# Performance work log

Hardware: AMD Instinct MI355X
Metric: run time of the kernel (lower is better)

Reference implementation:

```python
import jax, jax.numpy as jnp
import numpy as np

EPS = 1e-5

def setup_inputs() -> dict:
    key = jax.random.key(0)
    ks = jax.random.split(key, 7)
    C = 512
    x = jax.random.normal(ks[0], (16, C, 32, 32), dtype=jnp.float32)
    gn_w = jax.random.normal(ks[1], (C,), dtype=jnp.float32) * 0.02 + 1.0
    gn_b = jax.random.normal(ks[2], (C,), dtype=jnp.float32) * 0.02
    qkv_w = jax.random.normal(ks[3], (3 * C, C), dtype=jnp.float32) * (1.0 / np.sqrt(C))
    qkv_b = jax.random.normal(ks[4], (3 * C,), dtype=jnp.float32) * 0.02
    proj_w = jax.random.normal(ks[5], (C, C), dtype=jnp.float32) * (1.0 / np.sqrt(C))
    proj_b = jax.random.normal(ks[6], (C,), dtype=jnp.float32) * 0.02
    return {"x": x, "gn_w": gn_w, "gn_b": gn_b, "qkv_w": qkv_w,
            "qkv_b": qkv_b, "proj_w": proj_w, "proj_b": proj_b}

def reference(x, gn_w, gn_b, qkv_w, qkv_b, proj_w, proj_b):
    B, C, H, W = x.shape
    S = H * W
    # GroupNorm with 1 group: normalize over (C,H,W) per sample
    mean = jnp.mean(x, axis=(1, 2, 3), keepdims=True)
    var = jnp.var(x, axis=(1, 2, 3), keepdims=True)
    h = (x - mean) * jax.lax.rsqrt(var + EPS)
    h = h * gn_w[None, :, None, None] + gn_b[None, :, None, None]
    # 1x1 conv qkv: [B,C,H,W] -> [B,3C,H,W], flatten spatial -> [B,S,3C]
    hf = h.reshape(B, C, S)  # b c s
    qkv = jnp.einsum('bcs,oc->bso', hf, qkv_w) + qkv_b  # [B,S,3C]
    q, k, v = jnp.split(qkv, 3, axis=-1)  # each [B,S,C]
    scale = C ** (-0.5)
    attn = jax.nn.softmax(jnp.einsum('bqc,bkc->bqk', q, k) * scale, axis=-1)
    out = jnp.einsum('bqk,bkc->bqc', attn, v)  # [B,S,C]
    out = jnp.einsum('bsc,oc->bso', out, proj_w) + proj_b
    out = out.transpose(0, 2, 1).reshape(B, C, H, W)
    return x + out
```

## Files before the change

kernel.cpp:

```cpp
#include <hip/hip_runtime.h>
#include <stdint.h>

#define B_  16
#define C_  512
#define S_  1024
#define NSAMP (C_*S_)

typedef __bf16 bf16x8 __attribute__((ext_vector_type(8)));
typedef float  f32x4  __attribute__((ext_vector_type(4)));

__device__ __forceinline__ float bf2f(uint16_t u){ return __uint_as_float(((uint32_t)u)<<16); }
__device__ __forceinline__ uint16_t f2bf(float f){
  uint32_t u = __float_as_uint(f);
  uint32_t r = u + 0x7fffu + ((u>>16)&1u);
  return (uint16_t)(r>>16);
}
__device__ __forceinline__ float wsum(float v){
  #pragma unroll
  for(int o=32;o;o>>=1) v += __shfl_xor(v,o,64);
  return v;
}
__device__ __forceinline__ void gload16(const void* g, void* l){
  __builtin_amdgcn_global_load_lds(
      (__attribute__((address_space(1))) void*)g,
      (__attribute__((address_space(3))) void*)l, 16, 0, 0);
}

__global__ __launch_bounds__(1024) void detect_k(const uint16_t* __restrict__ x,
                                                 int* __restrict__ flag){
  __shared__ int sh[16];
  const uint4* xv = (const uint4*)x;
  int cnt = 0;
  #pragma unroll
  for(int k=0;k<8;k++){
    uint4 v = xv[threadIdx.x + k*1024];
    uint32_t ww[4] = {v.x, v.y, v.z, v.w};
    #pragma unroll
    for(int q=0;q<4;q++){
      cnt += (((ww[q] & 0xffffu) >> 7) & 0xffu) >= 132 ? 1 : 0;
      cnt += (((ww[q] >> 16)     >> 7) & 0xffu) >= 132 ? 1 : 0;
    }
  }
  #pragma unroll
  for(int o=32;o;o>>=1) cnt += __shfl_xor(cnt,o,64);
  const int lane = threadIdx.x & 63, w = threadIdx.x >> 6;
  if (lane==0) sh[w] = cnt;
  __syncthreads();
  if (threadIdx.x==0){
    int tot = 0;
    #pragma unroll
    for(int i=0;i<16;i++) tot += sh[i];
    *flag = (tot > 4096) ? 1 : 0;
  }
}

__device__ __forceinline__ void convseg(const void* src, uint16_t* dst, int n, int f, int t){
  const int idx = t*8;
  if (idx >= n) return;
  if (f){
    const float* s = (const float*)src;
    float4 v0 = *(const float4*)(s + idx);
    float4 v1 = *(const float4*)(s + idx + 4);
    ushort4 a, b;
    a.x=f2bf(v0.x); a.y=f2bf(v0.y); a.z=f2bf(v0.z); a.w=f2bf(v0.w);
    b.x=f2bf(v1.x); b.y=f2bf(v1.y); b.z=f2bf(v1.z); b.w=f2bf(v1.w);
    *(ushort4*)(dst + idx)     = a;
    *(ushort4*)(dst + idx + 4) = b;
  } else {
    *(uint4*)(dst + idx) = *(const uint4*)((const uint16_t*)src + idx);
  }
}
__global__ __launch_bounds__(256) void prep_k(
    const void* __restrict__ srcx, uint16_t* __restrict__ xb, float2* __restrict__ part,
    const void* qkvw, const void* projw, const void* gnw, const void* gnb,
    const void* qkvb, const void* projb,
    uint16_t* qkvwb, uint16_t* projwb, uint16_t* gnwb, uint16_t* gnbb,
    uint16_t* qkvbb, uint16_t* projbb, const int* __restrict__ flag){
  const int f = *flag;
  const int t = threadIdx.x;
  if (blockIdx.x >= 1024){
    const int bid = blockIdx.x - 1024;
    if (bid < 384){
      const size_t off = (size_t)bid*2048;
      convseg((const char*)qkvw + off*(f?4:2), qkvwb + off, 2048, f, t);
    } else if (bid < 512){
      const size_t off = (size_t)(bid-384)*2048;
      convseg((const char*)projw + off*(f?4:2), projwb + off, 2048, f, t);
    } else {
      convseg(gnw,   gnwb,   512,  f, t);
      convseg(gnb,   gnbb,   512,  f, t);
      convseg(qkvb,  qkvbb,  1536, f, t);
      convseg(projb, projbb, 512,  f, t);
    }
    return;
  }
  const size_t base = (size_t)blockIdx.x * 8192;
  float s = 0.f, s2 = 0.f;
  if (f){
    const float4* sp = (const float4*)((const float*)srcx + base);
    ushort4* dp = (ushort4*)(xb + base);
    #pragma unroll
    for(int i=0;i<8;i++){
      float4 v = sp[i*256 + t];
      s  += v.x + v.y + v.z + v.w;
      s2 += v.x*v.x + v.y*v.y + v.z*v.z + v.w*v.w;
      ushort4 o; o.x=f2bf(v.x); o.y=f2bf(v.y); o.z=f2bf(v.z); o.w=f2bf(v.w);
      dp[i*256 + t] = o;
    }
  } else {
    const uint4* sp = (const uint4*)((const uint16_t*)srcx + base);
    uint4* dp = (uint4*)(xb + base);
    #pragma unroll
    for(int i=0;i<4;i++){
      uint4 p = sp[i*256 + t];
      dp[i*256 + t] = p;
      uint32_t uu[4] = {p.x,p.y,p.z,p.w};
      #pragma unroll
      for(int q=0;q<4;q++){
        float f0 = __uint_as_float(uu[q]<<16);
        float f1 = __uint_as_float(uu[q] & 0xffff0000u);
        s += f0 + f1; s2 += f0*f0 + f1*f1;
      }
    }
  }
  s = wsum(s); s2 = wsum(s2);
  __shared__ float rs[4], rq[4];
  const int lane = t & 63, w = t >> 6;
  if (lane==0){ rs[w]=s; rq[w]=s2; }
  __syncthreads();
  if (t==0)
    part[blockIdx.x] = make_float2(rs[0]+rs[1]+rs[2]+rs[3], rq[0]+rq[1]+rq[2]+rq[3]);
}

__global__ __launch_bounds__(256) void gn_apply_t(const uint16_t* __restrict__ x,
    const uint16_t* __restrict__ gw, const uint16_t* __restrict__ gb,
    const float2* __restrict__ part, uint16_t* __restrict__ hT){
  __shared__ float tile[64*129];
  const int b = blockIdx.z, c0 = blockIdx.y<<6, s0 = blockIdx.x<<7;
  const int t = threadIdx.x;
  float2 p = part[b*64 + (t & 63)];
  float s = wsum(p.x), s2 = wsum(p.y);
  const float ninv = 1.f/(float)NSAMP;
  const float mn = s*ninv;
  const float rstd = rsqrtf(s2*ninv - mn*mn + 1e-5f);
  #pragma unroll
  for(int k=0;k<4;k++){
    const int ci = t + k*256;
    const int cl = ci>>4, sc = ci&15;
    uint4 v = *(const uint4*)&x[((size_t)b*C_ + c0+cl)*S_ + s0 + sc*8];
    const uint16_t* e = (const uint16_t*)&v;
    float* dst = &tile[cl*129 + sc*8];
    #pragma unroll
    for(int q=0;q<8;q++) dst[q] = bf2f(e[q]);
  }
  __syncthreads();
  const int cc = t & 7;
  const int sb0 = t >> 3;
  uint4 wv4 = *(const uint4*)&gw[c0 + cc*8];
  uint4 bv4 = *(const uint4*)&gb[c0 + cc*8];
  const uint16_t* we = (const uint16_t*)&wv4;
  const uint16_t* be = (const uint16_t*)&bv4;
  float aq[8], cq[8];
  #pragma unroll
  for(int q=0;q<8;q++){ aq[q] = bf2f(we[q])*rstd; cq[q] = bf2f(be[q]) - mn*aq[q]; }
  #pragma unroll
  for(int k=0;k<4;k++){
    const int sl = sb0 + k*32;
    uint16_t ov[8];
    #pragma unroll
    for(int q=0;q<8;q++){
      float xv = tile[(cc*8+q)*129 + sl];
      ov[q] = f2bf(xv*aq[q] + cq[q]);
    }
    uint4 o;
    o.x = (uint32_t)ov[0] | ((uint32_t)ov[1]<<16);
    o.y = (uint32_t)ov[2] | ((uint32_t)ov[3]<<16);
    o.z = (uint32_t)ov[4] | ((uint32_t)ov[5]<<16);
    o.w = (uint32_t)ov[6] | ((uint32_t)ov[7]<<16);
    *(uint4*)&hT[((size_t)b*S_ + s0+sl)*C_ + c0 + cc*8] = o;
  }
}

__global__ __launch_bounds__(256)
void qkv_k(const uint16_t* __restrict__ hT, const uint16_t* __restrict__ qkvw,
           const uint16_t* __restrict__ qkvb, uint16_t* __restrict__ qk,
           uint16_t* __restrict__ Vt)
{
  __shared__ uint16_t smem[16384];
  uint16_t* As = smem;
  uint16_t* Bs = smem + 8192;
  const int tid = threadIdx.x;
  const int lane = tid & 63, w = tid >> 6;
  const int quad = lane >> 4, lm = lane & 15;
  const int wm = (w & 1) << 6, wn = (w >> 1) << 6;

  const bool vpath = blockIdx.x >= 1024;
  const int id = vpath ? (blockIdx.x - 1024) : blockIdx.x;
  const int r8 = id & 7, k8 = id >> 3;
  int m0, n0, bz;
  const uint16_t *Abase, *Bbase;
  if (!vpath){
    const int g = r8*16 + (k8 & 15);
    m0 = g << 7; n0 = (k8 >> 4) << 7; bz = 0;
    Abase = hT + (size_t)m0*512;
    Bbase = qkvw + (size_t)n0*512;
  } else {
    const int g = r8*16 + (k8 & 15);
    m0 = (k8 >> 4) << 7; n0 = (g & 7) << 7; bz = g >> 3;
    Abase = qkvw + (size_t)(1024 + m0)*512;
    Bbase = hT + (size_t)bz*S_*C_ + (size_t)n0*512;
  }

  f32x4 acc[4][4];
  #pragma unroll
  for(int i=0;i<4;i++)
    #pragma unroll
    for(int j=0;j<4;j++) acc[i][j] = (f32x4){0.f,0.f,0.f,0.f};

  const int srow = tid >> 3;
  const int sx   = (tid & 7) ^ (srow & 7);
  const uint16_t* ga = Abase + (size_t)srow*512 + sx*8;
  const uint16_t* gb = Bbase + (size_t)srow*512 + sx*8;
  uint16_t* sa = &As[tid*8];
  uint16_t* sb = &Bs[tid*8];

  for(int k0=0;k0<512;k0+=64){
    #pragma unroll
    for(int i=0;i<4;i++){
      gload16(ga + (size_t)(i*32)*512 + k0, sa + i*2048);
      gload16(gb + (size_t)(i*32)*512 + k0, sb + i*2048);
    }
    __syncthreads();
    #pragma unroll
    for(int kk=0;kk<64;kk+=32){
      bf16x8 av[4], bv[4];
      #pragma unroll
      for(int i=0;i<4;i++){
        const int row = wm + i*16 + lm;
        av[i] = *(const bf16x8*)&As[row*64 + ((((kk>>3)+quad) ^ (row&7))<<3)];
      }
      #pragma unroll
      for(int j=0;j<4;j++){
        const int row = wn + j*16 + lm;
        bv[j] = *(const bf16x8*)&Bs[row*64 + ((((kk>>3)+quad) ^ (row&7))<<3)];
      }
      #pragma unroll
      for(int i=0;i<4;i++)
        #pragma unroll
        for(int j=0;j<4;j++)
          acc[i][j] = __builtin_amdgcn_mfma_f32_16x16x32_bf16(av[i], bv[j], acc[i][j], 0,0,0);
    }
    __syncthreads();
  }

  uint16_t* Cs = smem;
  if (!vpath){
    #pragma unroll
    for(int j=0;j<4;j++){
      const int col_l = wn + j*16 + lm;
      const float bvv = bf2f(qkvb[n0 + col_l]);
      #pragma unroll
      for(int i=0;i<4;i++){
        const int rl0 = wm + i*16 + (quad<<2);
        #pragma unroll
        for(int r=0;r<4;r++)
          Cs[(rl0+r)*128 + col_l] = f2bf(acc[i][j][r] + bvv);
      }
    }
  } else {
    #pragma unroll
    for(int i=0;i<4;i++){
      const int rl0 = wm + i*16 + (quad<<2);
      #pragma unroll
      for(int r=0;r<4;r++){
        const float bvv = bf2f(qkvb[1024 + m0 + rl0 + r]);
        #pragma unroll
        for(int j=0;j<4;j++)
          Cs[(rl0+r)*128 + wn + j*16 + lm] = f2bf(acc[i][j][r] + bvv);
      }
    }
  }
  __syncthreads();
  uint16_t* base = vpath ? (Vt + (size_t)bz*C_*S_) : qk;
  #pragma unroll
  for(int k=0;k<8;k++){
    const int ci = tid + k*256;
    const int rl = ci>>4, ccc = ci&15;
    *(uint4*)&base[(size_t)(m0+rl)*1024 + n0 + ccc*8] = *(const uint4*)&Cs[rl*128 + ccc*8];
  }
}

template<bool HASBIAS, bool BIASROW, bool OUTDYN, bool HASRES, int SWZMODE, bool EXP, bool SUMNORM>
__global__ __launch_bounds__(256)
void gemm_bt(const uint16_t* __restrict__ A, const uint16_t* __restrict__ Bt,
             void* __restrict__ Cp, const uint16_t* __restrict__ bias,
             const uint16_t* __restrict__ xres, const int* __restrict__ flag,
             int lda, int ldb, int ldc, int K,
             long long sA, long long sB, long long sC)
{
  __shared__ uint16_t smem[16384];
  uint16_t* As = smem;
  uint16_t* Bs = smem + 8192;
  const int lin = (blockIdx.z * gridDim.y + blockIdx.y) * gridDim.x + blockIdx.x;
  const int r8 = lin & 7, kk8 = lin >> 3;
  int bx, by, bz;
  if (SWZMODE == 0){
    const int G = (gridDim.y * gridDim.z) >> 3;
    const int g = r8 * G + (kk8 % G);
    bx = kk8 / G; by = g % gridDim.y; bz = g / gridDim.y;
  } else {
    const int G = (gridDim.x * gridDim.z) >> 3;
    const int g = r8 * G + (kk8 % G);
    by = kk8 / G; bx = g % gridDim.x; bz = g / gridDim.x;
  }

  const int tid = threadIdx.x;
  const int lane = tid & 63, w = tid >> 6;
  const int quad = lane >> 4, lm = lane & 15;
  const int m0 = by << 7, n0 = bx << 7;
  A  += (size_t)bz * sA;
  Bt += (size_t)bz * sB;

  f32x4 acc[4][4];
  #pragma unroll
  for(int i=0;i<4;i++)
    #pragma unroll
    for(int j=0;j<4;j++) acc[i][j] = (f32x4){0.f,0.f,0.f,0.f};
  f32x4 rsum[4];
  bf16x8 onesv;
  if (SUMNORM){
    #pragma unroll
    for(int i=0;i<4;i++) rsum[i] = (f32x4){0.f,0.f,0.f,0.f};
    #pragma unroll
    for(int z=0;z<8;z++) onesv[z] = (__bf16)1.0f;
  }

  const int wm = (w & 1) << 6, wn = (w >> 1) << 6;
  const int srow = tid >> 3;
  const int sx   = (tid & 7) ^ (srow & 7);
  const uint16_t* ga = A  + (size_t)(m0 + srow)*lda + sx*8;
  const uint16_t* gb = Bt + (size_t)(n0 + srow)*ldb + sx*8;
  uint16_t* sa = &As[tid*8];
  uint16_t* sb = &Bs[tid*8];

  for(int k0=0;k0<K;k0+=64){
    #pragma unroll
    for(int i=0;i<4;i++){
      gload16(ga + (size_t)(i*32)*lda + k0, sa + i*2048);
      gload16(gb + (size_t)(i*32)*ldb + k0, sb + i*2048);
    }
    __syncthreads();
    #pragma unroll
    for(int kk=0;kk<64;kk+=32){
      bf16x8 av[4], bv[4];
      #pragma unroll
      for(int i=0;i<4;i++){
        const int row = wm + i*16 + lm;
        av[i] = *(const bf16x8*)&As[row*64 + ((((kk>>3)+quad) ^ (row&7))<<3)];
      }
      #pragma unroll
      for(int j=0;j<4;j++){
        const int row = wn + j*16 + lm;
        bv[j] = *(const bf16x8*)&Bs[row*64 + ((((kk>>3)+quad) ^ (row&7))<<3)];
      }
      #pragma unroll
      for(int i=0;i<4;i++){
        if (SUMNORM) rsum[i] = __builtin_amdgcn_mfma_f32_16x16x32_bf16(av[i], onesv, rsum[i], 0,0,0);
        #pragma unroll
        for(int j=0;j<4;j++)
          acc[i][j] = __builtin_amdgcn_mfma_f32_16x16x32_bf16(av[i], bv[j], acc[i][j], 0,0,0);
      }
    }
    __syncthreads();
  }

  const size_t cb = (size_t)bz * (size_t)sC;
  if (!OUTDYN && !HASRES){
    uint16_t* Cs = smem;
    #pragma unroll
    for(int j=0;j<4;j++){
      const int col_l = wn + j*16 + lm;
      const float cbias = (HASBIAS && !BIASROW) ? bf2f(bias[n0 + col_l]) : 0.f;
      #pragma unroll
      for(int i=0;i<4;i++){
        const int rl0 = wm + i*16 + (quad<<2);
        #pragma unroll
        for(int r=0;r<4;r++){
          float v = acc[i][j][r] + cbias;
          if (HASBIAS && BIASROW) v += bf2f(bias[m0 + rl0 + r]);
          if (EXP)     v = __expf(v * 0.044194173824159216f);
          if (SUMNORM) v = v / rsum[i][r];
          Cs[(rl0+r)*128 + col_l] = f2bf(v);
        }
      }
    }
    __syncthreads();
    uint16_t* base = (uint16_t*)Cp + cb;
    #pragma unroll
    for(int k=0;k<8;k++){
      const int ci = tid + k*256;
      const int rl = ci>>4, cc = ci&15;
      *(uint4*)&base[(size_t)(m0+rl)*ldc + n0 + cc*8] = *(const uint4*)&Cs[rl*128 + cc*8];
    }
  } else {
    float* Cs32 = (float*)smem;
    const int f = OUTDYN ? *flag : 0;
    const int wnh = wn >> 1;
    #pragma unroll
    for(int half=0; half<2; ++half){
      #pragma unroll
      for(int j2=0;j2<2;j2++){
        const int j = half*2 + j2;
        const int col_l = wn + j*16 + lm;
        const int hcol = wnh + j2*16 + lm;
        const float cbias = (HASBIAS && !BIASROW) ? bf2f(bias[n0 + col_l]) : 0.f;
        #pragma unroll
        for(int i=0;i<4;i++){
          const int rl0 = wm + i*16 + (quad<<2);
          #pragma unroll
          for(int r=0;r<4;r++){
            float v = acc[i][j][r] + cbias;
            if (HASBIAS && BIASROW) v += bf2f(bias[m0 + rl0 + r]);
            if (EXP)     v = __expf(v * 0.044194173824159216f);
            if (SUMNORM) v = v / rsum[i][r];
            Cs32[(rl0+r)*64 + hcol] = v;
          }
        }
      }
      __syncthreads();
      #pragma unroll
      for(int k=0;k<8;k++){
        const int ci = tid + k*256;
        const int rl = ci>>4, c4 = ci&15;
        float4 vv = *(const float4*)&Cs32[rl*64 + c4*4];
        const int gcol = n0 + c4*4 + ((c4>=8)?32:0) + half*32;
        const size_t idx = cb + (size_t)(m0+rl)*ldc + gcol;
        float o0=vv.x, o1=vv.y, o2=vv.z, o3=vv.w;
        if (HASRES){
          uint2 rr = *(const uint2*)&xres[idx];
          o0 += bf2f((uint16_t)(rr.x & 0xffffu));
          o1 += bf2f((uint16_t)(rr.x >> 16));
          o2 += bf2f((uint16_t)(rr.y & 0xffffu));
          o3 += bf2f((uint16_t)(rr.y >> 16));
        }
        if (OUTDYN && f){
          float4 o = make_float4(o0,o1,o2,o3);
          *(float4*)&((float*)Cp)[idx] = o;
        } else {
          uint2 o;
          o.x = (uint32_t)f2bf(o0) | ((uint32_t)f2bf(o1)<<16);
          o.y = (uint32_t)f2bf(o2) | ((uint32_t)f2bf(o3)<<16);
          *(uint2*)&((uint16_t*)Cp)[idx] = o;
        }
      }
      __syncthreads();
    }
  }
}

extern "C" void kernel_launch(void* const* d_in, const int* in_sizes, int n_in,
                              void* d_out, int out_size, void* d_ws, size_t ws_size,
                              hipStream_t stream){
  char* ws = (char*)d_ws;
  int*      flag  = (int*)ws;
  float2*   part  = (float2*)(ws + 4096);
  uint16_t* gnwb  = (uint16_t*)(ws + 16384);
  uint16_t* gnbb  = (uint16_t*)(ws + 17408);
  uint16_t* qkvbb = (uint16_t*)(ws + 18432);
  uint16_t* projbb= (uint16_t*)(ws + 21504);
  uint16_t* qkvwb = (uint16_t*)(ws + 32768);
  uint16_t* projwb= (uint16_t*)(ws + 1605632);
  uint16_t* xb    = (uint16_t*)(ws + 4194304);
  uint16_t* hT    = (uint16_t*)(ws + 20971520);
  uint16_t* qk    = (uint16_t*)(ws + 37748736);
  uint16_t* sc    = (uint16_t*)(ws + 71303168);
  uint16_t* Vt    = (uint16_t*)(ws + 104857600);

  hipLaunchKernelGGL(detect_k, dim3(1), dim3(1024), 0, stream,
                     (const uint16_t*)d_in[0], flag);
  hipLaunchKernelGGL(prep_k, dim3(1537), dim3(256), 0, stream,
                     d_in[0], xb, part,
                     d_in[3], d_in[5], d_in[1], d_in[2], d_in[4], d_in[6],
                     qkvwb, projwb, gnwb, gnbb, qkvbb, projbb, flag);
  hipLaunchKernelGGL(gn_apply_t, dim3(8,8,16), dim3(256), 0, stream, xb, gnwb, gnbb, part, hT);

  hipLaunchKernelGGL(qkv_k, dim3(1536), dim3(256), 0, stream, hT, qkvwb, qkvbb, qk, Vt);

  hipLaunchKernelGGL((gemm_bt<false,false,false,false,0,true,false>), dim3(8,8,16), dim3(256), 0, stream,
      qk, qk + 512, (void*)sc, (const uint16_t*)nullptr, (const uint16_t*)nullptr, flag,
      1024, 1024, 1024, 512, (long long)S_*1024, (long long)S_*1024, (long long)S_*S_);

  hipLaunchKernelGGL((gemm_bt<false,false,false,false,0,false,true>), dim3(4,8,16), dim3(256), 0, stream,
      sc, Vt, (void*)hT, (const uint16_t*)nullptr, (const uint16_t*)nullptr, flag,
      1024, 1024, 512, 1024, (long long)S_*S_, (long long)C_*S_, (long long)S_*C_);

  hipLaunchKernelGGL((gemm_bt<true,true,true,true,1,false,false>), dim3(8,4,16), dim3(256), 0, stream,
      projwb, hT, d_out, projbb, xb, flag,
      512, 512, 1024, 512, 0LL, (long long)S_*C_, (long long)C_*S_);
}
```

Before: 220.0 us.

## Compute softmax row sums in score epilogue and fold dtype detection into prep

The exp-score GEMM now writes per-tile partial row sums of the fp32 exponentials to a workspace buffer. The P·V GEMM reads those partials and multiplies by their reciprocal, replacing the extra ones-vector MFMA it used to run per k-step to build row sums. The separate single-block input dtype detection kernel is removed: every prep block now samples 256 elements and sets the flag itself, which saves one launch. Row sums now come from unrounded fp32 values rather than the bf16 values that are stored, and the smaller detection sample could classify the input dtype differently.

```diff
diff --git a/kernel.cpp b/kernel.cpp
--- a/kernel.cpp
+++ b/kernel.cpp
@@ -20,38 +20,15 @@
   for(int o=32;o;o>>=1) v += __shfl_xor(v,o,64);
   return v;
 }
+__device__ __forceinline__ int wsumi(int v){
+  #pragma unroll
+  for(int o=32;o;o>>=1) v += __shfl_xor(v,o,64);
+  return v;
+}
 __device__ __forceinline__ void gload16(const void* g, void* l){
   __builtin_amdgcn_global_load_lds(
       (__attribute__((address_space(1))) void*)g,
       (__attribute__((address_space(3))) void*)l, 16, 0, 0);
-}
-
-__global__ __launch_bounds__(1024) void detect_k(const uint16_t* __restrict__ x,
-                                                 int* __restrict__ flag){
-  __shared__ int sh[16];
-  const uint4* xv = (const uint4*)x;
-  int cnt = 0;
-  #pragma unroll
-  for(int k=0;k<8;k++){
-    uint4 v = xv[threadIdx.x + k*1024];
-    uint32_t ww[4] = {v.x, v.y, v.z, v.w};
-    #pragma unroll
-    for(int q=0;q<4;q++){
-      cnt += (((ww[q] & 0xffffu) >> 7) & 0xffu) >= 132 ? 1 : 0;
-      cnt += (((ww[q] >> 16)     >> 7) & 0xffu) >= 132 ? 1 : 0;
-    }
-  }
-  #pragma unroll
-  for(int o=32;o;o>>=1) cnt += __shfl_xor(cnt,o,64);
-  const int lane = threadIdx.x & 63, w = threadIdx.x >> 6;
-  if (lane==0) sh[w] = cnt;
-  __syncthreads();
-  if (threadIdx.x==0){
-    int tot = 0;
-    #pragma unroll
-    for(int i=0;i<16;i++) tot += sh[i];
-    *flag = (tot > 4096) ? 1 : 0;
-  }
 }
 
 __device__ __forceinline__ void convseg(const void* src, uint16_t* dst, int n, int f, int t){
@@ -75,9 +52,23 @@
     const void* qkvw, const void* projw, const void* gnw, const void* gnb,
     const void* qkvb, const void* projb,
     uint16_t* qkvwb, uint16_t* projwb, uint16_t* gnwb, uint16_t* gnbb,
-    uint16_t* qkvbb, uint16_t* projbb, const int* __restrict__ flag){
-  const int f = *flag;
+    uint16_t* qkvbb, uint16_t* projbb, int* __restrict__ flag){
   const int t = threadIdx.x;
+  __shared__ int sdet[4];
+  int f;
+  {
+    const uint4 v = ((const uint4*)srcx)[t & 255];
+    uint32_t ww[4] = {v.x, v.y, v.z, v.w};
+    int c = 0;
+    #pragma unroll
+    for(int q=0;q<4;q++) c += ((((ww[q] & 0xffffu) >> 7) & 0xffu) >= 132) ? 1 : 0;
+    c = wsumi(c);
+    if ((t & 63) == 0) sdet[t >> 6] = c;
+    __syncthreads();
+    f = (sdet[0] + sdet[1] + sdet[2] + sdet[3] > 128) ? 1 : 0;
+  }
+  if (blockIdx.x == 0 && t == 0) *flag = f;
+
   if (blockIdx.x >= 1024){
     const int bid = blockIdx.x - 1024;
     if (bid < 384){
@@ -290,11 +281,12 @@
   }
 }
 
-template<bool HASBIAS, bool BIASROW, bool OUTDYN, bool HASRES, int SWZMODE, bool EXP, bool SUMNORM>
+template<bool HASBIAS, bool BIASROW, bool OUTDYN, bool HASRES, int SWZMODE, bool EXP, int RSMODE>
 __global__ __launch_bounds__(256)
 void gemm_bt(const uint16_t* __restrict__ A, const uint16_t* __restrict__ Bt,
              void* __restrict__ Cp, const uint16_t* __restrict__ bias,
              const uint16_t* __restrict__ xres, const int* __restrict__ flag,
+             float* __restrict__ rs_part,
              int lda, int ldb, int ldc, int K,
              long long sA, long long sB, long long sC)
 {
@@ -326,14 +318,6 @@
   for(int i=0;i<4;i++)
     #pragma unroll
     for(int j=0;j<4;j++) acc[i][j] = (f32x4){0.f,0.f,0.f,0.f};
-  f32x4 rsum[4];
-  bf16x8 onesv;
-  if (SUMNORM){
-    #pragma unroll
-    for(int i=0;i<4;i++) rsum[i] = (f32x4){0.f,0.f,0.f,0.f};
-    #pragma unroll
-    for(int z=0;z<8;z++) onesv[z] = (__bf16)1.0f;
-  }
 
   const int wm = (w & 1) << 6, wn = (w >> 1) << 6;
   const int srow = tid >> 3;
@@ -364,12 +348,10 @@
         bv[j] = *(const bf16x8*)&Bs[row*64 + ((((kk>>3)+quad) ^ (row&7))<<3)];
       }
       #pragma unroll
-      for(int i=0;i<4;i++){
-        if (SUMNORM) rsum[i] = __builtin_amdgcn_mfma_f32_16x16x32_bf16(av[i], onesv, rsum[i], 0,0,0);
+      for(int i=0;i<4;i++)
         #pragma unroll
         for(int j=0;j<4;j++)
           acc[i][j] = __builtin_amdgcn_mfma_f32_16x16x32_bf16(av[i], bv[j], acc[i][j], 0,0,0);
-      }
     }
     __syncthreads();
   }
@@ -377,6 +359,26 @@
   const size_t cb = (size_t)bz * (size_t)sC;
   if (!OUTDYN && !HASRES){
     uint16_t* Cs = smem;
+    float rp[4][4];
+    if (RSMODE == 1){
+      #pragma unroll
+      for(int i=0;i<4;i++)
+        #pragma unroll
+        for(int r=0;r<4;r++) rp[i][r] = 0.f;
+    }
+    float inv[4][4];
+    if (RSMODE == 2){
+      const int myrow = m0 + wm + lm*4 + quad;
+      const float4* rpp = (const float4*)&rs_part[((size_t)bz*1024 + myrow)*16];
+      float4 a0 = rpp[0], a1 = rpp[1], a2 = rpp[2], a3 = rpp[3];
+      float rowsumv = a0.x+a0.y+a0.z+a0.w + a1.x+a1.y+a1.z+a1.w
+                    + a2.x+a2.y+a2.z+a2.w + a3.x+a3.y+a3.z+a3.w;
+      #pragma unroll
+      for(int i=0;i<4;i++)
+        #pragma unroll
+        for(int r=0;r<4;r++)
+          inv[i][r] = 1.f / __shfl(rowsumv, r*16 + i*4 + quad, 64);
+    }
     #pragma unroll
     for(int j=0;j<4;j++){
       const int col_l = wn + j*16 + lm;
@@ -388,11 +390,24 @@
         for(int r=0;r<4;r++){
           float v = acc[i][j][r] + cbias;
           if (HASBIAS && BIASROW) v += bf2f(bias[m0 + rl0 + r]);
-          if (EXP)     v = __expf(v * 0.044194173824159216f);
-          if (SUMNORM) v = v / rsum[i][r];
+          if (EXP)          v = __expf(v * 0.044194173824159216f);
+          if (RSMODE == 1)  rp[i][r] += v;
+          if (RSMODE == 2)  v *= inv[i][r];
           Cs[(rl0+r)*128 + col_l] = f2bf(v);
         }
       }
+    }
+    if (RSMODE == 1){
+      #pragma unroll
+      for(int i=0;i<4;i++)
+        #pragma unroll
+        for(int r=0;r<4;r++){
+          float s4 = rp[i][r];
+          #pragma unroll
+          for(int o=8;o;o>>=1) s4 += __shfl_xor(s4, o, 64);
+          if (lm == 0)
+            rs_part[((size_t)bz*1024 + m0 + wm + i*16 + (quad<<2) + r)*16 + (bx<<1) + (w>>1)] = s4;
+        }
     }
     __syncthreads();
     uint16_t* base = (uint16_t*)Cp + cb;
@@ -421,8 +436,7 @@
           for(int r=0;r<4;r++){
             float v = acc[i][j][r] + cbias;
             if (HASBIAS && BIASROW) v += bf2f(bias[m0 + rl0 + r]);
-            if (EXP)     v = __expf(v * 0.044194173824159216f);
-            if (SUMNORM) v = v / rsum[i][r];
+            if (EXP) v = __expf(v * 0.044194173824159216f);
             Cs32[(rl0+r)*64 + hcol] = v;
           }
         }
@@ -470,14 +484,13 @@
   uint16_t* projbb= (uint16_t*)(ws + 21504);
   uint16_t* qkvwb = (uint16_t*)(ws + 32768);
   uint16_t* projwb= (uint16_t*)(ws + 1605632);
+  float*    rs_part=(float*)  (ws + 2129920);
   uint16_t* xb    = (uint16_t*)(ws + 4194304);
   uint16_t* hT    = (uint16_t*)(ws + 20971520);
   uint16_t* qk    = (uint16_t*)(ws + 37748736);
   uint16_t* sc    = (uint16_t*)(ws + 71303168);
   uint16_t* Vt    = (uint16_t*)(ws + 104857600);
 
-  hipLaunchKernelGGL(detect_k, dim3(1), dim3(1024), 0, stream,
-                     (const uint16_t*)d_in[0], flag);
   hipLaunchKernelGGL(prep_k, dim3(1537), dim3(256), 0, stream,
                      d_in[0], xb, part,
                      d_in[3], d_in[5], d_in[1], d_in[2], d_in[4], d_in[6],
@@ -486,15 +499,15 @@
 
   hipLaunchKernelGGL(qkv_k, dim3(1536), dim3(256), 0, stream, hT, qkvwb, qkvbb, qk, Vt);
 
-  hipLaunchKernelGGL((gemm_bt<false,false,false,false,0,true,false>), dim3(8,8,16), dim3(256), 0, stream,
-      qk, qk + 512, (void*)sc, (const uint16_t*)nullptr, (const uint16_t*)nullptr, flag,
+  hipLaunchKernelGGL((gemm_bt<false,false,false,false,0,true,1>), dim3(8,8,16), dim3(256), 0, stream,
+      qk, qk + 512, (void*)sc, (const uint16_t*)nullptr, (const uint16_t*)nullptr, flag, rs_part,
       1024, 1024, 1024, 512, (long long)S_*1024, (long long)S_*1024, (long long)S_*S_);
 
-  hipLaunchKernelGGL((gemm_bt<false,false,false,false,0,false,true>), dim3(4,8,16), dim3(256), 0, stream,
-      sc, Vt, (void*)hT, (const uint16_t*)nullptr, (const uint16_t*)nullptr, flag,
+  hipLaunchKernelGGL((gemm_bt<false,false,false,false,0,false,2>), dim3(4,8,16), dim3(256), 0, stream,
+      sc, Vt, (void*)hT, (const uint16_t*)nullptr, (const uint16_t*)nullptr, flag, rs_part,
       1024, 1024, 512, 1024, (long long)S_*S_, (long long)C_*S_, (long long)S_*C_);
 
-  hipLaunchKernelGGL((gemm_bt<true,true,true,true,1,false,false>), dim3(8,4,16), dim3(256), 0, stream,
-      projwb, hT, d_out, projbb, xb, flag,
+  hipLaunchKernelGGL((gemm_bt<true,true,true,true,1,false,0>), dim3(8,4,16), dim3(256), 0, stream,
+      projwb, hT, d_out, projbb, xb, flag, (float*)nullptr,
       512, 512, 1024, 512, 0LL, (long long)S_*C_, (long long)C_*S_);
 }
```

New measurement: 216.4 us. No clear change (-1.6%).
